# Performance work log

Hardware: AMD Instinct MI355X
Metric: run time of the kernel (lower is better)

The kernel has to match this reference:

```python
import jax, jax.numpy as jnp
import numpy as np

NUM_NODES = 1024
K = 16384
G = 128

def setup_inputs() -> dict:
    key = jax.random.key(0)
    k1, k2, k3 = jax.random.split(key, 3)
    x = jax.random.normal(k1, (G, NUM_NODES, 64), dtype=jnp.float32)
    # original draws fresh xavier-uniform embeddings inside forward; we
    # materialize equivalent random embeddings here (only ordering matters).
    emb_s = jax.random.normal(k2, (G, NUM_NODES, 1), dtype=jnp.float32)
    emb_t = jax.random.normal(k3, (G, 1, NUM_NODES), dtype=jnp.float32)
    return {"x": x, "emb_s": emb_s, "emb_t": emb_t}

def reference(x, emb_s, emb_t):
    num_graphs = x.shape[0]
    n = NUM_NODES
    # rank-1 outer product adjacency: [G, N, N]
    adj = emb_s * emb_t  # broadcast (G,N,1)*(G,1,N)
    # mask diagonal with -inf
    diag = jnp.eye(n, dtype=bool)
    adj = jnp.where(diag[None, :, :], -jnp.inf, adj)
    # global top-k over flattened N*N per graph
    adj_flat = adj.reshape(num_graphs, n * n)
    _, indices = jax.lax.top_k(adj_flat, K)  # [G, K]
    # scatter ones at selected positions
    out_flat = jnp.zeros((num_graphs, n * n), dtype=adj.dtype)
    rows = jnp.arange(num_graphs)[:, None]
    out_flat = out_flat.at[rows, indices].set(1.0)
    return out_flat.reshape(num_graphs, n, n)
```

## Files before the change

### kernel.cpp

```cpp
#include <hip/hip_runtime.h>
#include <stdint.h>

#define NNODES 1024
#define NGRAPH 128
#define TOPK   16384
#define EQCAP  4096

typedef float vfloat4 __attribute__((ext_vector_type(4)));

__device__ __forceinline__ uint32_t fkey(float x) {
    uint32_t u = __float_as_uint(x);
    return (u & 0x80000000u) ? ~u : (u | 0x80000000u);
}
__device__ __forceinline__ float inv_fkey(uint32_t k) {
    uint32_t u = (k & 0x80000000u) ? (k & 0x7FFFFFFFu) : ~k;
    return __uint_as_float(u);
}
__device__ __forceinline__ void wavefence() {
    __builtin_amdgcn_wave_barrier();
    asm volatile("" ::: "memory");
}
__device__ __forceinline__ uint32_t wave_sum_dpp(uint32_t v) {
    int x = (int)v;
    x += __builtin_amdgcn_update_dpp(0, x, 0x111, 0xF, 0xF, true);
    x += __builtin_amdgcn_update_dpp(0, x, 0x112, 0xF, 0xF, true);
    x += __builtin_amdgcn_update_dpp(0, x, 0x114, 0xF, 0xF, true);
    x += __builtin_amdgcn_update_dpp(0, x, 0x118, 0xF, 0xF, true);
    x += __builtin_amdgcn_update_dpp(0, x, 0x142, 0xF, 0xF, true);
    x += __builtin_amdgcn_update_dpp(0, x, 0x143, 0xF, 0xF, true);
    return (uint32_t)x;
}

__global__ __launch_bounds__(NNODES)
void select_kernel(const float* __restrict__ s, const float* __restrict__ t,
                   uint32_t* __restrict__ Tout, uint32_t* __restrict__ Rout,
                   uint32_t* __restrict__ eqCntG, uint32_t* __restrict__ eqIdxG) {
    const int g = blockIdx.x, i = threadIdx.x;
    __shared__ uint64_t spk[NNODES];
    __shared__ float    tvs[NNODES];
    __shared__ uint32_t wsum[16], wsum2[16];
    __shared__ uint32_t sLo, sHi, sDir, sEqCnt;
    __shared__ uint32_t sEqList[EQCAP];

    const float tv_i = t[g * NNODES + i];
    spk[i] = ((uint64_t)fkey(tv_i) << 16) | (uint32_t)i;
    if (i == 0) sEqCnt = 0u;

    for (int k = 2; k <= NNODES; k <<= 1) {
        for (int j = k >> 1; j > 0; j >>= 1) {
            if ((j >= 64) || (j == 32 && k > 64)) __syncthreads();
            else                                  wavefence();
            int partner = i ^ j;
            if (partner > i) {
                bool asc = ((i & k) == 0);
                uint64_t a = spk[i], b = spk[partner];
                if ((a > b) == asc) { spk[i] = b; spk[partner] = a; }
            }
        }
    }
    __syncthreads();
    tvs[i] = inv_fkey((uint32_t)(spk[i] >> 16));

    const float sv = s[g * NNODES + i];
    const bool sneg = (__float_as_uint(sv) >> 31) != 0;
    const uint32_t kdiag = fkey(sv * tv_i);
    __syncthreads();

    {
        uint32_t m = fkey(sv * tvs[sneg ? 0 : (NNODES - 1)]);
        uint32_t n = fkey(sv * tvs[sneg ? 16 : (NNODES - 17)]);
        for (int off = 32; off; off >>= 1) {
            uint32_t mm = __shfl_down(m, off); if (mm > m) m = mm;
            uint32_t nn = __shfl_down(n, off); if (nn < n) n = nn;
        }
        if ((i & 63) == 0) { wsum[i >> 6] = m; wsum2[i >> 6] = n; }
        __syncthreads();
        if (i == 0) {
            uint32_t ub = 0u, lb = 0xFFFFFFFFu;
            for (int w = 0; w < 16; ++w) {
                if (wsum[w]  > ub) ub = wsum[w];
                if (wsum2[w] < lb) lb = wsum2[w];
            }
            sLo = lb; sHi = ub;
        }
        __syncthreads();
    }

    auto srchRange = [&](uint32_t cand, int lo_, int hi_) -> int {
        while (lo_ < hi_) {
            int mid = (lo_ + hi_) >> 1;
            bool pred = fkey(sv * tvs[mid]) > cand;
            bool goLeft = sneg ? !pred : pred;
            if (goLeft) hi_ = mid; else lo_ = mid + 1;
        }
        return lo_;
    };

    int rlo = 0, rhi = NNODES;
    uint32_t cntHi = 0u;

    for (int it = 0; it < 33; ++it) {
        const uint32_t lo = sLo, hi = sHi;
        if (lo >= hi) break;
        const uint32_t mid = lo + ((hi - lo) >> 1);
        const int b = srchRange(mid, rlo, rhi);
        uint32_t c = sneg ? (uint32_t)b : (uint32_t)(NNODES - b);
        if (kdiag > mid) c--;
        uint32_t r = wave_sum_dpp(c);
        if ((i & 63) == 63) wsum[i >> 6] = r;
        __syncthreads();
        if (i == 0) {
            uint32_t tot = 0;
            for (int w = 0; w < 16; ++w) tot += wsum[w];
            if (tot < TOPK) { sHi = mid; sDir = 0u; cntHi = tot; }
            else            { sLo = mid + 1; sDir = 1u; }
        }
        __syncthreads();
        if (sDir == 0u) { if (!sneg) rhi = b; else rlo = b; }
        else            { if (!sneg) rlo = b; else rhi = b; }
    }
    const uint32_t T = sLo;
    if (i == 0) { Tout[g] = T; Rout[g] = TOPK - cntHi; }

    auto bound = [&](bool ge) -> int {
        int lo_ = 0, hi_ = NNODES;
        while (lo_ < hi_) {
            int mid = (lo_ + hi_) >> 1;
            uint32_t k = fkey(sv * tvs[mid]);
            bool pred = ge ? (k >= T) : (k > T);
            bool goLeft = sneg ? !pred : pred;
            if (goLeft) hi_ = mid; else lo_ = mid + 1;
        }
        return lo_;
    };
    int e0, e1;
    if (!sneg) { e0 = bound(true);  e1 = bound(false); }
    else       { e0 = bound(false); e1 = bound(true);  }
    for (int p = e0; p < e1; ++p) {
        uint32_t j = (uint32_t)(spk[p] & 0xFFFFu);
        if ((int)j == i) continue;
        uint32_t slot = atomicAdd(&sEqCnt, 1u);
        if (slot < EQCAP) sEqList[slot] = (uint32_t)(i * NNODES) + j;
    }
    __syncthreads();
    uint32_t E = sEqCnt; if (E > EQCAP) E = EQCAP;
    if (i == 0) eqCntG[g] = E;
    for (uint32_t p = i; p < E; p += NNODES) eqIdxG[g * EQCAP + p] = sEqList[p];
}

__global__ __launch_bounds__(256)
void write_kernel(const float* __restrict__ s, const float* __restrict__ t,
                  const uint32_t* __restrict__ Tin, const uint32_t* __restrict__ Rin,
                  const uint32_t* __restrict__ eqCntG, const uint32_t* __restrict__ eqIdxG,
                  float* __restrict__ out) {
    const int b = blockIdx.x;
    const int g = b >> 10, i = b & 1023;
    const uint32_t T = Tin[g];
    const float sv = s[(size_t)g * NNODES + i];
    const vfloat4 tv = ((const vfloat4*)(t + (size_t)g * NNODES))[threadIdx.x];
    const int j0 = threadIdx.x * 4;
    const uint32_t k0 = fkey(sv * tv.x), k1 = fkey(sv * tv.y);
    const uint32_t k2 = fkey(sv * tv.z), k3 = fkey(sv * tv.w);
    vfloat4 o;
    o.x = (k0 > T && (j0 + 0) != i) ? 1.0f : 0.0f;
    o.y = (k1 > T && (j0 + 1) != i) ? 1.0f : 0.0f;
    o.z = (k2 > T && (j0 + 2) != i) ? 1.0f : 0.0f;
    o.w = (k3 > T && (j0 + 3) != i) ? 1.0f : 0.0f;
    if (k0 == T || k1 == T || k2 == T || k3 == T) {
        uint32_t E = eqCntG[g]; if (E > EQCAP) E = EQCAP;
        const uint32_t R = Rin[g];
        const uint32_t* eq = eqIdxG + (size_t)g * EQCAP;
        const uint32_t kk[4] = {k0, k1, k2, k3};
        #pragma unroll
        for (int q = 0; q < 4; ++q) {
            const uint32_t j = j0 + q;
            if (kk[q] == T && (int)j != i) {
                const uint32_t f = (uint32_t)i * NNODES + j;
                uint32_t rank = 0;
                for (uint32_t e2 = 0; e2 < E; ++e2) rank += (eq[e2] < f) ? 1u : 0u;
                if (rank < R) ((float*)&o)[q] = 1.0f;
            }
        }
    }
    ((vfloat4*)(out + (size_t)g * NNODES * NNODES + (size_t)i * NNODES))[threadIdx.x] = o;
}

extern "C" void kernel_launch(void* const* d_in, const int* in_sizes, int n_in,
                              void* d_out, int out_size, void* d_ws, size_t ws_size,
                              hipStream_t stream) {
    const float* s = (const float*)d_in[1];
    const float* t = (const float*)d_in[2];
    float* out = (float*)d_out;

    char* ws = (char*)d_ws;
    uint32_t* Tbuf  = (uint32_t*)ws; ws += (size_t)NGRAPH * 4;
    uint32_t* Rbuf  = (uint32_t*)ws; ws += (size_t)NGRAPH * 4;
    uint32_t* eqCnt = (uint32_t*)ws; ws += (size_t)NGRAPH * 4;
    uint32_t* eqIdx = (uint32_t*)ws; ws += (size_t)NGRAPH * EQCAP * 4;

    select_kernel<<<NGRAPH, NNODES, 0, stream>>>(s, t, Tbuf, Rbuf, eqCnt, eqIdx);
    write_kernel<<<NGRAPH * NNODES, 256, 0, stream>>>(s, t, Tbuf, Rbuf, eqCnt, eqIdx, out);
}
```

Measured before the change: 129.9 us.

## Replace binary threshold search with 4-ary search using one barrier per step

The threshold search in the select kernel changes from a 33-step binary search with two block barriers per step to a 17-step quaternary search. Each step tests three candidates with nested per-row binary searches. Wave partial counts are combined with shared-memory atomics into a triple-buffered counter array, so every thread reads the totals and updates its own bounds after a single barrier, with no thread-0 decision pass. This cuts barrier and serial latency in the one-block-per-graph kernel. In exchange, each thread does more search work per step and the code relies on the rotating buffers to avoid read/reset races.

```diff
diff --git a/kernel.cpp b/kernel.cpp
--- a/kernel.cpp
+++ b/kernel.cpp
@@ -39,12 +39,14 @@
     __shared__ uint64_t spk[NNODES];
     __shared__ float    tvs[NNODES];
     __shared__ uint32_t wsum[16], wsum2[16];
-    __shared__ uint32_t sLo, sHi, sDir, sEqCnt;
+    __shared__ uint32_t sCnt[3][3];
+    __shared__ uint32_t sLo, sHi, sEqCnt;
     __shared__ uint32_t sEqList[EQCAP];
 
     const float tv_i = t[g * NNODES + i];
     spk[i] = ((uint64_t)fkey(tv_i) << 16) | (uint32_t)i;
     if (i == 0) sEqCnt = 0u;
+    if (i < 3) { sCnt[i][0] = 0u; sCnt[i][1] = 0u; sCnt[i][2] = 0u; }
 
     for (int k = 2; k <= NNODES; k <<= 1) {
         for (int j = k >> 1; j > 0; j >>= 1) {
@@ -96,30 +98,58 @@
         return lo_;
     };
 
+    uint32_t lo = sLo, hi = sHi;
+    uint32_t cntHi = 0u;
     int rlo = 0, rhi = NNODES;
-    uint32_t cntHi = 0u;
-
-    for (int it = 0; it < 33; ++it) {
-        const uint32_t lo = sLo, hi = sHi;
+    for (int it = 0; it < 17; ++it) {
         if (lo >= hi) break;
-        const uint32_t mid = lo + ((hi - lo) >> 1);
-        const int b = srchRange(mid, rlo, rhi);
-        uint32_t c = sneg ? (uint32_t)b : (uint32_t)(NNODES - b);
-        if (kdiag > mid) c--;
-        uint32_t r = wave_sum_dpp(c);
-        if ((i & 63) == 63) wsum[i >> 6] = r;
+        const uint32_t range = hi - lo;
+        const uint32_t c0 = lo + (uint32_t)(((uint64_t)range * 1) >> 2);
+        const uint32_t c1 = lo + (uint32_t)(((uint64_t)range * 2) >> 2);
+        const uint32_t c2 = lo + (uint32_t)(((uint64_t)range * 3) >> 2);
+        int b0, b1, b2;
+        if (!sneg) {
+            b0 = srchRange(c0, rlo, rhi);
+            b1 = srchRange(c1, b0,  rhi);
+            b2 = srchRange(c2, b1,  rhi);
+        } else {
+            b0 = srchRange(c0, rlo, rhi);
+            b1 = srchRange(c1, rlo, b0);
+            b2 = srchRange(c2, rlo, b1);
+        }
+        uint32_t n0 = sneg ? (uint32_t)b0 : (uint32_t)(NNODES - b0);
+        uint32_t n1 = sneg ? (uint32_t)b1 : (uint32_t)(NNODES - b1);
+        uint32_t n2 = sneg ? (uint32_t)b2 : (uint32_t)(NNODES - b2);
+        if (kdiag > c0) n0--;
+        if (kdiag > c1) n1--;
+        if (kdiag > c2) n2--;
+        const uint32_t r0 = wave_sum_dpp(n0);
+        const uint32_t r1 = wave_sum_dpp(n1);
+        const uint32_t r2 = wave_sum_dpp(n2);
+        uint32_t* buf = sCnt[it % 3];
+        if ((i & 63) == 63) {
+            atomicAdd(&buf[0], r0);
+            atomicAdd(&buf[1], r1);
+            atomicAdd(&buf[2], r2);
+        }
+        if (i == 0) {
+            uint32_t* nb = sCnt[(it + 1) % 3];
+            nb[0] = 0u; nb[1] = 0u; nb[2] = 0u;
+        }
         __syncthreads();
-        if (i == 0) {
-            uint32_t tot = 0;
-            for (int w = 0; w < 16; ++w) tot += wsum[w];
-            if (tot < TOPK) { sHi = mid; sDir = 0u; cntHi = tot; }
-            else            { sLo = mid + 1; sDir = 1u; }
-        }
-        __syncthreads();
-        if (sDir == 0u) { if (!sneg) rhi = b; else rlo = b; }
-        else            { if (!sneg) rlo = b; else rhi = b; }
-    }
-    const uint32_t T = sLo;
+        const uint32_t t0 = buf[0], t1 = buf[1], t2 = buf[2];
+        if (t0 < TOPK)      { hi = c0; cntHi = t0;
+                              if (!sneg) rhi = b0; else rlo = b0; }
+        else if (t1 < TOPK) { lo = c0 + 1; hi = c1; cntHi = t1;
+                              if (!sneg) { rlo = b0; rhi = b1; }
+                              else       { rlo = b1; rhi = b0; } }
+        else if (t2 < TOPK) { lo = c1 + 1; hi = c2; cntHi = t2;
+                              if (!sneg) { rlo = b1; rhi = b2; }
+                              else       { rlo = b2; rhi = b1; } }
+        else                { lo = c2 + 1;
+                              if (!sneg) rlo = b2; else rhi = b2; }
+    }
+    const uint32_t T = lo;
     if (i == 0) { Tout[g] = T; Rout[g] = TOPK - cntHi; }
 
     auto bound = [&](bool ge) -> int {
```

Result: slower. 143.0 us (+10.1%).
